# Kernel tuning notes

Hardware: AMD Instinct MI355X
Metric: run time of the kernel (lower is better)

The kernel has to match this reference:

```python
import jax, jax.numpy as jnp
import numpy as np

SMOOTHING = 0.9  # NEURON_CONFIG['signal_smoothing']
NUM_SOURCE = 16384
NUM_TARGET = 16384
NUM_BRANCHES = 64
BATCH = 32


def setup_inputs() -> dict:
    key = jax.random.key(0)
    k1, k2, k3, k4 = jax.random.split(key, 4)
    spikes = jax.random.normal(k1, (BATCH, NUM_SOURCE), dtype=jnp.float32)
    attenuation = jax.random.uniform(k2, (NUM_SOURCE, NUM_BRANCHES), dtype=jnp.float32)
    target_indices = jax.random.randint(k3, (NUM_SOURCE, NUM_BRANCHES), 0, NUM_TARGET)
    delays = jax.random.randint(k4, (NUM_SOURCE, NUM_BRANCHES), 0, 6)
    return {"spikes": spikes, "attenuation": attenuation,
            "target_indices": target_indices, "delays": delays}


def reference(spikes, attenuation, target_indices, delays):
    # spikes: [B, S]; attenuation/delays/target_indices: [S, Br]
    B = spikes.shape[0]
    num_target = NUM_TARGET
    att = jnp.clip(attenuation, 0.0, 1.0)
    decay = SMOOTHING ** delays.astype(spikes.dtype)          # [S, Br]
    # fused elementwise: signal per (batch, source, branch)
    signals = spikes[:, :, None] * (att * decay)[None, :, :]   # [B, S, Br]
    flat_t = target_indices.reshape(-1)                        # [S*Br]
    flat_s = signals.reshape(B, -1)                            # [B, S*Br]
    out = jnp.zeros((B, num_target), dtype=spikes.dtype)
    out = out.at[jnp.arange(B)[:, None], flat_t[None, :]].add(flat_s)
    return out
```

## Files before the change

### kernel.cpp

```cpp
#include <hip/hip_runtime.h>

#define S_   16384
#define T_   16384
#define B_   32
#define NEDGES (S_ * 64)
#define GP_  256
#define EPG  4096
#define NBKT 512
#define TPB  32
#define CAP_SRT 2560

__device__ __forceinline__ float edge_weight(float a, int d) {
  float w = fminf(fmaxf(a, 0.0f), 1.0f);
  float r = (d & 1) ? 0.9f : 1.0f;
  r = (d & 2) ? r * 0.81f   : r;
  r = (d & 4) ? r * 0.6561f : r;
  return w * r;
}

__global__ __launch_bounds__(1024) void produce(
    const float* __restrict__ spikes,
    const float* __restrict__ att,
    const int*   __restrict__ tgt,
    const int*   __restrict__ del,
    float*        __restrict__ spikesT,
    int2*         __restrict__ rec,
    unsigned int* __restrict__ ofse) {
  __shared__ float tile[64][33];
  __shared__ int4  sbuf4[EPG / 2];
  __shared__ int   cnt5[NBKT], cur5[NBKT], sofs5[NBKT];
  __shared__ int   wtot[8];
  int2* buf = (int2*)sbuf4;

  const int g   = blockIdx.x;
  const int tid = threadIdx.x;
  if (tid < NBKT) cnt5[tid] = 0;

  const int s0 = g * 64;
  {
    const int x = tid & 63, y = tid >> 6;
    tile[x][y]      = spikes[(size_t)y        * S_ + s0 + x];
    tile[x][y + 16] = spikes[(size_t)(y + 16) * S_ + s0 + x];
  }

  const int e4  = g * 1024 + tid;
  int4   t = reinterpret_cast<const int4*>(tgt)[e4];
  float4 a = reinterpret_cast<const float4*>(att)[e4];
  int4   d = reinterpret_cast<const int4*>(del)[e4];
  const int src = (e4 * 4) >> 6;

  __syncthreads();

  {
    const int b = tid & 31, j = tid >> 5;
    spikesT[(size_t)(s0 + j)      * 32 + b] = tile[j][b];
    spikesT[(size_t)(s0 + j + 32) * 32 + b] = tile[j + 32][b];
  }

  const int bk0 = t.x >> 5, bk1 = t.y >> 5, bk2 = t.z >> 5, bk3 = t.w >> 5;
  __hip_atomic_fetch_add(&cnt5[bk0], 1, __ATOMIC_RELAXED, __HIP_MEMORY_SCOPE_WORKGROUP);
  __hip_atomic_fetch_add(&cnt5[bk1], 1, __ATOMIC_RELAXED, __HIP_MEMORY_SCOPE_WORKGROUP);
  __hip_atomic_fetch_add(&cnt5[bk2], 1, __ATOMIC_RELAXED, __HIP_MEMORY_SCOPE_WORKGROUP);
  __hip_atomic_fetch_add(&cnt5[bk3], 1, __ATOMIC_RELAXED, __HIP_MEMORY_SCOPE_WORKGROUP);
  __syncthreads();

  int v = 0, incl = 0;
  if (tid < NBKT) {
    v = cnt5[tid];
    incl = v;
#pragma unroll
    for (int off = 1; off < 64; off <<= 1) {
      int u = __shfl_up(incl, off);
      if ((tid & 63) >= off) incl += u;
    }
    if ((tid & 63) == 63) wtot[tid >> 6] = incl;
  }
  __syncthreads();
  if (tid < NBKT) {
    int base = 0;
    const int wv = tid >> 6;
    for (int i = 0; i < wv; ++i) base += wtot[i];
    const int start = base + incl - v;
    sofs5[tid] = start;
    cur5[tid]  = start;
  }
  __syncthreads();

#define PUT(BK, TL, AV, DV)                                                   \
  {                                                                           \
    int p = __hip_atomic_fetch_add(&cur5[BK], 1, __ATOMIC_RELAXED,            \
                                   __HIP_MEMORY_SCOPE_WORKGROUP);             \
    buf[p] = make_int2(((TL) << 14) | src,                                    \
                       __float_as_int(edge_weight((AV), (DV))));              \
  }
  PUT(bk0, t.x & 31, a.x, d.x)
  PUT(bk1, t.y & 31, a.y, d.y)
  PUT(bk2, t.z & 31, a.z, d.z)
  PUT(bk3, t.w & 31, a.w, d.w)
#undef PUT
  __syncthreads();

  int4* recO = reinterpret_cast<int4*>(rec) + (size_t)g * (EPG / 2);
  recO[tid]        = sbuf4[tid];
  recO[tid + 1024] = sbuf4[tid + 1024];
  if (tid < NBKT)
    ofse[(size_t)g * NBKT + tid] =
        ((unsigned)cur5[tid] << 16) | (unsigned)sofs5[tid];
}

__global__ __launch_bounds__(512) void consume(
    const int2*  __restrict__ rec,
    const unsigned int* __restrict__ ofse,
    const float* __restrict__ spikesT,
    float* __restrict__ out) {
  __shared__ int2  raw[CAP_SRT];
  __shared__ int2  srt[CAP_SRT];
  __shared__ float otile[TPB][33];
  __shared__ unsigned sse[GP_];
  __shared__ int   sstart[GP_];
  __shared__ int   wtot4[4];
  __shared__ int   h32[TPB], ofs[TPB + 1], cur32[TPB];

  const int k   = blockIdx.x;
  const int tid = threadIdx.x;
  const int b   = tid & 31;
  const int hw  = tid >> 5;

  if (tid < TPB) h32[tid] = 0;
  if (tid < GP_) sse[tid] = ofse[(size_t)tid * NBKT + k];
  __syncthreads();

  int v = 0, incl = 0;
  if (tid < GP_) {
    const unsigned u = sse[tid];
    v = (int)(u >> 16) - (int)(u & 0xFFFF);
    incl = v;
#pragma unroll
    for (int off = 1; off < 64; off <<= 1) {
      int uu = __shfl_up(incl, off);
      if ((tid & 63) >= off) incl += uu;
    }
    if ((tid & 63) == 63) wtot4[tid >> 6] = incl;
  }
  __syncthreads();
  if (tid < GP_) {
    int base = 0;
    const int wv = tid >> 6;
    for (int i = 0; i < wv; ++i) base += wtot4[i];
    sstart[tid] = base + incl - v;
  }
  __syncthreads();
  const int total = min(wtot4[0] + wtot4[1] + wtot4[2] + wtot4[3], CAP_SRT);

  for (int it = 0; it < 16; ++it) {
    const int g = hw + it * 16;
    const unsigned u = sse[g];
    const int st = (int)(u & 0xFFFF);
    const int n  = (int)(u >> 16) - st;
    const int2* slice = rec + (size_t)g * EPG + st;
    const int lbase = sstart[g];
    for (int j = b; j < n; j += 32) {
      int2 r = slice[j];
      __hip_atomic_fetch_add(&h32[(r.x >> 14) & 31], 1, __ATOMIC_RELAXED,
                             __HIP_MEMORY_SCOPE_WORKGROUP);
      const int idx = lbase + j;
      if (idx < CAP_SRT) raw[idx] = r;
    }
  }
  __syncthreads();

  if (tid < 32) {
    int vv = h32[tid], ii = vv;
#pragma unroll
    for (int off = 1; off < 32; off <<= 1) {
      int uu = __shfl_up(ii, off);
      if (tid >= off) ii += uu;
    }
    ofs[tid]   = ii - vv;
    cur32[tid] = ii - vv;
    if (tid == 31) ofs[32] = ii;
  }
  __syncthreads();

  for (int i = tid; i < total; i += 512) {
    int2 r = raw[i];
    int p = __hip_atomic_fetch_add(&cur32[(r.x >> 14) & 31], 1,
                                   __ATOMIC_RELAXED,
                                   __HIP_MEMORY_SCOPE_WORKGROUP);
    if (p < CAP_SRT) srt[p] = r;
  }
  __syncthreads();

  float acc0 = 0.f, acc1 = 0.f;
  {
    int e        = ofs[hw];
    const int e1 = min(ofs[hw + 1], total);
    for (; e + 4 <= e1; e += 4) {
      int2 r0 = srt[e], r1 = srt[e + 1], r2 = srt[e + 2], r3 = srt[e + 3];
      float s0 = spikesT[(size_t)(r0.x & 0x3FFF) * 32 + b];
      float s1 = spikesT[(size_t)(r1.x & 0x3FFF) * 32 + b];
      float s2 = spikesT[(size_t)(r2.x & 0x3FFF) * 32 + b];
      float s3 = spikesT[(size_t)(r3.x & 0x3FFF) * 32 + b];
      acc0 = fmaf(__int_as_float(r0.y), s0, acc0);
      acc0 = fmaf(__int_as_float(r1.y), s1, acc0);
      acc0 = fmaf(__int_as_float(r2.y), s2, acc0);
      acc0 = fmaf(__int_as_float(r3.y), s3, acc0);
    }
    for (; e < e1; ++e) {
      int2 r = srt[e];
      acc0 = fmaf(__int_as_float(r.y), spikesT[(size_t)(r.x & 0x3FFF) * 32 + b], acc0);
    }
  }
  {
    int e        = ofs[hw + 16];
    const int e1 = min(ofs[hw + 17], total);
    for (; e + 4 <= e1; e += 4) {
      int2 r0 = srt[e], r1 = srt[e + 1], r2 = srt[e + 2], r3 = srt[e + 3];
      float s0 = spikesT[(size_t)(r0.x & 0x3FFF) * 32 + b];
      float s1 = spikesT[(size_t)(r1.x & 0x3FFF) * 32 + b];
      float s2 = spikesT[(size_t)(r2.x & 0x3FFF) * 32 + b];
      float s3 = spikesT[(size_t)(r3.x & 0x3FFF) * 32 + b];
      acc1 = fmaf(__int_as_float(r0.y), s0, acc1);
      acc1 = fmaf(__int_as_float(r1.y), s1, acc1);
      acc1 = fmaf(__int_as_float(r2.y), s2, acc1);
      acc1 = fmaf(__int_as_float(r3.y), s3, acc1);
    }
    for (; e < e1; ++e) {
      int2 r = srt[e];
      acc1 = fmaf(__int_as_float(r.y), spikesT[(size_t)(r.x & 0x3FFF) * 32 + b], acc1);
    }
  }

  otile[hw][b]      = acc0;
  otile[hw + 16][b] = acc1;
  __syncthreads();
  const int bb = tid >> 4;
  const int cc = (tid & 15) * 2;
  float2 o2 = make_float2(otile[cc][bb], otile[cc + 1][bb]);
  *reinterpret_cast<float2*>(&out[(size_t)bb * T_ + k * 32 + cc]) = o2;
}

__global__ void zero_floats(float* __restrict__ p, int n) {
  int i = blockIdx.x * blockDim.x + threadIdx.x;
  if (i < n) p[i] = 0.0f;
}

__global__ void naive_kernel(const float* __restrict__ spikes,
                             const float* __restrict__ att,
                             const int*   __restrict__ tgt,
                             const int*   __restrict__ del,
                             float*       __restrict__ out) {
  int i = blockIdx.x * blockDim.x + threadIdx.x;
  if (i >= NEDGES) return;
  int   s = i >> 6;
  int   t = tgt[i];
  float w = edge_weight(att[i], del[i]);
  for (int b = 0; b < B_; ++b)
    unsafeAtomicAdd(&out[(size_t)b * T_ + t], w * spikes[(size_t)b * S_ + s]);
}

extern "C" void kernel_launch(void* const* d_in, const int* in_sizes, int n_in,
                              void* d_out, int out_size, void* d_ws, size_t ws_size,
                              hipStream_t stream) {
  const float* spikes = (const float*)d_in[0];
  const float* att    = (const float*)d_in[1];
  const int*   tgt    = (const int*)d_in[2];
  const int*   del    = (const int*)d_in[3];
  float*       out    = (float*)d_out;

  const size_t spikesT_bytes = (size_t)S_ * B_ * sizeof(float);
  const size_t rec_bytes     = (size_t)NEDGES * sizeof(int2);
  const size_t ofse_bytes    = (size_t)GP_ * NBKT * sizeof(unsigned);
  const size_t need = spikesT_bytes + rec_bytes + ofse_bytes + 64;

  if (ws_size < need) {
    zero_floats<<<(B_ * T_ + 255) / 256, 256, 0, stream>>>(out, B_ * T_);
    naive_kernel<<<(NEDGES + 255) / 256, 256, 0, stream>>>(spikes, att, tgt, del, out);
    return;
  }

  char* p = (char*)d_ws;
  float*        spikesT = (float*)p;        p += spikesT_bytes;
  int2*         rec     = (int2*)p;         p += rec_bytes;
  unsigned int* ofse    = (unsigned int*)p;

  produce<<<GP_, 1024, 0, stream>>>(spikes, att, tgt, del, spikesT, rec, ofse);
  consume<<<NBKT, 512, 0, stream>>>(rec, ofse, spikesT, out);
}
```

Baseline: 93.87 us.

## Halve producer groups, transpose offset table, gather bucket records into registers

The producer now runs twice as many smaller groups (512 threads, 2048 edges each), and a new transpose kernel reorders the per-group bucket offset table so the consumer reads its 512 entries contiguously instead of with a large stride. In the consumer, the prefix scan over groups and the raw staging buffer are removed. Each lane instead loads up to one record per group into registers and pushes any overflow into a small shared stash before the counting sort. This cuts strided global reads and shared-memory staging, at the cost of an extra kernel launch and the risk of dropping records if the stash overflows.

```diff
diff --git a/kernel.cpp b/kernel.cpp
--- a/kernel.cpp
+++ b/kernel.cpp
@@ -4,11 +4,12 @@
 #define T_   16384
 #define B_   32
 #define NEDGES (S_ * 64)
-#define GP_  256
-#define EPG  4096
+#define GP_  512
+#define EPG  2048
 #define NBKT 512
 #define TPB  32
-#define CAP_SRT 2560
+#define CAP_SRT   2560
+#define CAP_STASH 512
 
 __device__ __forceinline__ float edge_weight(float a, int d) {
   float w = fminf(fmaxf(a, 0.0f), 1.0f);
@@ -18,7 +19,7 @@
   return w * r;
 }
 
-__global__ __launch_bounds__(1024) void produce(
+__global__ __launch_bounds__(512) void produce(
     const float* __restrict__ spikes,
     const float* __restrict__ att,
     const int*   __restrict__ tgt,
@@ -26,7 +27,7 @@
     float*        __restrict__ spikesT,
     int2*         __restrict__ rec,
     unsigned int* __restrict__ ofse) {
-  __shared__ float tile[64][33];
+  __shared__ float tile[32][33];
   __shared__ int4  sbuf4[EPG / 2];
   __shared__ int   cnt5[NBKT], cur5[NBKT], sofs5[NBKT];
   __shared__ int   wtot[8];
@@ -34,27 +35,27 @@
 
   const int g   = blockIdx.x;
   const int tid = threadIdx.x;
-  if (tid < NBKT) cnt5[tid] = 0;
-
-  const int s0 = g * 64;
-  {
-    const int x = tid & 63, y = tid >> 6;
+  cnt5[tid] = 0;
+
+  const int s0 = g * 32;
+  {
+    const int x = tid & 31, y = tid >> 5;
     tile[x][y]      = spikes[(size_t)y        * S_ + s0 + x];
     tile[x][y + 16] = spikes[(size_t)(y + 16) * S_ + s0 + x];
   }
 
-  const int e4  = g * 1024 + tid;
+  const int e4  = g * 512 + tid;
   int4   t = reinterpret_cast<const int4*>(tgt)[e4];
   float4 a = reinterpret_cast<const float4*>(att)[e4];
   int4   d = reinterpret_cast<const int4*>(del)[e4];
-  const int src = (e4 * 4) >> 6;
+  const int src = e4 >> 4;
 
   __syncthreads();
 
   {
     const int b = tid & 31, j = tid >> 5;
     spikesT[(size_t)(s0 + j)      * 32 + b] = tile[j][b];
-    spikesT[(size_t)(s0 + j + 32) * 32 + b] = tile[j + 32][b];
+    spikesT[(size_t)(s0 + j + 16) * 32 + b] = tile[j + 16][b];
   }
 
   const int bk0 = t.x >> 5, bk1 = t.y >> 5, bk2 = t.z >> 5, bk3 = t.w >> 5;
@@ -64,19 +65,16 @@
   __hip_atomic_fetch_add(&cnt5[bk3], 1, __ATOMIC_RELAXED, __HIP_MEMORY_SCOPE_WORKGROUP);
   __syncthreads();
 
-  int v = 0, incl = 0;
-  if (tid < NBKT) {
-    v = cnt5[tid];
-    incl = v;
+  int v = cnt5[tid];
+  int incl = v;
 #pragma unroll
-    for (int off = 1; off < 64; off <<= 1) {
-      int u = __shfl_up(incl, off);
-      if ((tid & 63) >= off) incl += u;
-    }
-    if ((tid & 63) == 63) wtot[tid >> 6] = incl;
-  }
-  __syncthreads();
-  if (tid < NBKT) {
+  for (int off = 1; off < 64; off <<= 1) {
+    int u = __shfl_up(incl, off);
+    if ((tid & 63) >= off) incl += u;
+  }
+  if ((tid & 63) == 63) wtot[tid >> 6] = incl;
+  __syncthreads();
+  {
     int base = 0;
     const int wv = tid >> 6;
     for (int i = 0; i < wv; ++i) base += wtot[i];
@@ -101,70 +99,71 @@
   __syncthreads();
 
   int4* recO = reinterpret_cast<int4*>(rec) + (size_t)g * (EPG / 2);
-  recO[tid]        = sbuf4[tid];
-  recO[tid + 1024] = sbuf4[tid + 1024];
-  if (tid < NBKT)
-    ofse[(size_t)g * NBKT + tid] =
-        ((unsigned)cur5[tid] << 16) | (unsigned)sofs5[tid];
+  recO[tid]       = sbuf4[tid];
+  recO[tid + 512] = sbuf4[tid + 512];
+  ofse[(size_t)g * NBKT + tid] =
+      ((unsigned)cur5[tid] << 16) | (unsigned)sofs5[tid];
+}
+
+__global__ __launch_bounds__(256) void transpose_ofse(
+    const unsigned int* __restrict__ in, unsigned int* __restrict__ out) {
+  __shared__ unsigned tl[32][33];
+  const int x = threadIdx.x, y = threadIdx.y;
+  const int r0 = blockIdx.y * 32, c0 = blockIdx.x * 32;
+  for (int i = y; i < 32; i += 8)
+    tl[i][x] = in[(size_t)(r0 + i) * NBKT + c0 + x];
+  __syncthreads();
+  for (int i = y; i < 32; i += 8)
+    out[(size_t)(c0 + i) * GP_ + r0 + x] = tl[x][i];
 }
 
 __global__ __launch_bounds__(512) void consume(
     const int2*  __restrict__ rec,
-    const unsigned int* __restrict__ ofse,
+    const unsigned int* __restrict__ ofseT,
     const float* __restrict__ spikesT,
     float* __restrict__ out) {
-  __shared__ int2  raw[CAP_SRT];
   __shared__ int2  srt[CAP_SRT];
+  __shared__ int2  stash[CAP_STASH];
   __shared__ float otile[TPB][33];
   __shared__ unsigned sse[GP_];
-  __shared__ int   sstart[GP_];
-  __shared__ int   wtot4[4];
   __shared__ int   h32[TPB], ofs[TPB + 1], cur32[TPB];
+  __shared__ int   stash_n;
 
   const int k   = blockIdx.x;
   const int tid = threadIdx.x;
   const int b   = tid & 31;
   const int hw  = tid >> 5;
+  const int sub = (b >> 3);
+  const int j   = b & 7;
 
   if (tid < TPB) h32[tid] = 0;
-  if (tid < GP_) sse[tid] = ofse[(size_t)tid * NBKT + k];
-  __syncthreads();
-
-  int v = 0, incl = 0;
-  if (tid < GP_) {
-    const unsigned u = sse[tid];
-    v = (int)(u >> 16) - (int)(u & 0xFFFF);
-    incl = v;
+  if (tid == 0)  stash_n = 0;
+  sse[tid] = ofseT[(size_t)k * GP_ + tid];
+  __syncthreads();
+
+  int2 rr[8];
+  int  rv = 0;
 #pragma unroll
-    for (int off = 1; off < 64; off <<= 1) {
-      int uu = __shfl_up(incl, off);
-      if ((tid & 63) >= off) incl += uu;
-    }
-    if ((tid & 63) == 63) wtot4[tid >> 6] = incl;
-  }
-  __syncthreads();
-  if (tid < GP_) {
-    int base = 0;
-    const int wv = tid >> 6;
-    for (int i = 0; i < wv; ++i) base += wtot4[i];
-    sstart[tid] = base + incl - v;
-  }
-  __syncthreads();
-  const int total = min(wtot4[0] + wtot4[1] + wtot4[2] + wtot4[3], CAP_SRT);
-
-  for (int it = 0; it < 16; ++it) {
-    const int g = hw + it * 16;
+  for (int it = 0; it < 8; ++it) {
+    const int g = it * 64 + hw * 4 + sub;
     const unsigned u = sse[g];
     const int st = (int)(u & 0xFFFF);
     const int n  = (int)(u >> 16) - st;
     const int2* slice = rec + (size_t)g * EPG + st;
-    const int lbase = sstart[g];
-    for (int j = b; j < n; j += 32) {
+    if (j < n) {
       int2 r = slice[j];
       __hip_atomic_fetch_add(&h32[(r.x >> 14) & 31], 1, __ATOMIC_RELAXED,
                              __HIP_MEMORY_SCOPE_WORKGROUP);
-      const int idx = lbase + j;
-      if (idx < CAP_SRT) raw[idx] = r;
+      rr[it] = r;
+      rv |= 1 << it;
+    }
+    for (int j2 = j + 8; j2 < n; j2 += 8) {
+      int2 r = slice[j2];
+      __hip_atomic_fetch_add(&h32[(r.x >> 14) & 31], 1, __ATOMIC_RELAXED,
+                             __HIP_MEMORY_SCOPE_WORKGROUP);
+      int sp = __hip_atomic_fetch_add(&stash_n, 1, __ATOMIC_RELAXED,
+                                      __HIP_MEMORY_SCOPE_WORKGROUP);
+      if (sp < CAP_STASH) stash[sp] = r;
     }
   }
   __syncthreads();
@@ -182,8 +181,18 @@
   }
   __syncthreads();
 
-  for (int i = tid; i < total; i += 512) {
-    int2 r = raw[i];
+#pragma unroll
+  for (int it = 0; it < 8; ++it)
+    if (rv & (1 << it)) {
+      int2 r = rr[it];
+      int p = __hip_atomic_fetch_add(&cur32[(r.x >> 14) & 31], 1,
+                                     __ATOMIC_RELAXED,
+                                     __HIP_MEMORY_SCOPE_WORKGROUP);
+      if (p < CAP_SRT) srt[p] = r;
+    }
+  const int ns = min(stash_n, CAP_STASH);
+  for (int i = tid; i < ns; i += 512) {
+    int2 r = stash[i];
     int p = __hip_atomic_fetch_add(&cur32[(r.x >> 14) & 31], 1,
                                    __ATOMIC_RELAXED,
                                    __HIP_MEMORY_SCOPE_WORKGROUP);
@@ -194,7 +203,7 @@
   float acc0 = 0.f, acc1 = 0.f;
   {
     int e        = ofs[hw];
-    const int e1 = min(ofs[hw + 1], total);
+    const int e1 = min(ofs[hw + 1], CAP_SRT);
     for (; e + 4 <= e1; e += 4) {
       int2 r0 = srt[e], r1 = srt[e + 1], r2 = srt[e + 2], r3 = srt[e + 3];
       float s0 = spikesT[(size_t)(r0.x & 0x3FFF) * 32 + b];
@@ -213,7 +222,7 @@
   }
   {
     int e        = ofs[hw + 16];
-    const int e1 = min(ofs[hw + 17], total);
+    const int e1 = min(ofs[hw + 17], CAP_SRT);
     for (; e + 4 <= e1; e += 4) {
       int2 r0 = srt[e], r1 = srt[e + 1], r2 = srt[e + 2], r3 = srt[e + 3];
       float s0 = spikesT[(size_t)(r0.x & 0x3FFF) * 32 + b];
@@ -271,7 +280,7 @@
   const size_t spikesT_bytes = (size_t)S_ * B_ * sizeof(float);
   const size_t rec_bytes     = (size_t)NEDGES * sizeof(int2);
   const size_t ofse_bytes    = (size_t)GP_ * NBKT * sizeof(unsigned);
-  const size_t need = spikesT_bytes + rec_bytes + ofse_bytes + 64;
+  const size_t need = spikesT_bytes + rec_bytes + 2 * ofse_bytes + 64;
 
   if (ws_size < need) {
     zero_floats<<<(B_ * T_ + 255) / 256, 256, 0, stream>>>(out, B_ * T_);
@@ -282,8 +291,10 @@
   char* p = (char*)d_ws;
   float*        spikesT = (float*)p;        p += spikesT_bytes;
   int2*         rec     = (int2*)p;         p += rec_bytes;
-  unsigned int* ofse    = (unsigned int*)p;
-
-  produce<<<GP_, 1024, 0, stream>>>(spikes, att, tgt, del, spikesT, rec, ofse);
-  consume<<<NBKT, 512, 0, stream>>>(rec, ofse, spikesT, out);
-}
+  unsigned int* ofse    = (unsigned int*)p; p += ofse_bytes;
+  unsigned int* ofseT   = (unsigned int*)p;
+
+  produce<<<GP_, 512, 0, stream>>>(spikes, att, tgt, del, spikesT, rec, ofse);
+  transpose_ofse<<<dim3(NBKT / 32, GP_ / 32), dim3(32, 8), 0, stream>>>(ofse, ofseT);
+  consume<<<NBKT, 512, 0, stream>>>(rec, ofseT, spikesT, out);
+}
```

Measured after the change: 94.21 us. About the same (+0.4%).
